# Kernel optimization log

Measured on AMD Instinct MI355X. Metric: run time of the kernel, lower is better.

The kernel has to match this reference:

```python
import jax, jax.numpy as jnp
import numpy as np

H = 8
D_MODEL = 512
D_K = D_MODEL // H
NEG = -1e9


def setup_inputs() -> dict:
    key = jax.random.key(0)
    ks = jax.random.split(key, 11)
    B, S = 2, 2048
    scale = 1.0 / np.sqrt(D_MODEL)
    inp = {
        'query': jax.random.normal(ks[0], (B, S, D_MODEL), dtype=jnp.float32),
        'key': jax.random.normal(ks[1], (B, S, D_MODEL), dtype=jnp.float32),
        'value': jax.random.normal(ks[2], (B, S, D_MODEL), dtype=jnp.float32),
        'Wq': jax.random.normal(ks[3], (D_MODEL, D_MODEL), dtype=jnp.float32) * scale,
        'bq': jnp.zeros((D_MODEL,), dtype=jnp.float32),
        'Wk': jax.random.normal(ks[4], (D_MODEL, D_MODEL), dtype=jnp.float32) * scale,
        'bk': jnp.zeros((D_MODEL,), dtype=jnp.float32),
        'Wv': jax.random.normal(ks[5], (D_MODEL, D_MODEL), dtype=jnp.float32) * scale,
        'bv': jnp.zeros((D_MODEL,), dtype=jnp.float32),
        'Wo': jax.random.normal(ks[6], (D_MODEL, D_MODEL), dtype=jnp.float32) * scale,
        'bo': jnp.zeros((D_MODEL,), dtype=jnp.float32),
    }
    return inp


def reference(query, key, value, Wq, bq, Wk, bk, Wv, bv, Wo, bo):
    B, S, _ = query.shape
    # QKV projections (nn.Linear: x @ W.T + b), split into heads -> [B, H, S, D_K]
    def proj(x, W, b):
        return (x @ W.T + b).reshape(B, S, H, D_K).transpose(0, 2, 1, 3)

    q = proj(query, Wq, bq)
    k = proj(key, Wk, bk)
    v = proj(value, Wv, bv)

    scores = jnp.einsum('bhqd,bhkd->bhqk', q, k) / jnp.sqrt(jnp.float32(D_K))
    # diagonal mask (mask=True): token cannot attend to itself
    diag = jnp.eye(S, dtype=bool)
    scores = jnp.where(diag, NEG, scores)

    p_attn = jax.nn.softmax(scores, axis=-1)  # [B, H, S, S]
    x = jnp.einsum('bhqk,bhkd->bhqd', p_attn, v)
    x = x.transpose(0, 2, 1, 3).reshape(B, S, H * D_K)
    return x @ Wo.T + bo
```

## Files before the change

### kernel.cpp

```cpp
#include <hip/hip_runtime.h>
#include <hip/hip_bf16.h>
#include <math.h>

#define NUM_H 8
#define DK    64
#define DM    512
#define SEQ   2048
#define NB    2
#define MROWS (NB*SEQ)

typedef unsigned short u16;
typedef unsigned int   u32;
typedef __attribute__((ext_vector_type(8))) __bf16 bf16x8;
typedef __attribute__((ext_vector_type(4))) short  s16x4;
typedef __attribute__((ext_vector_type(4))) float  f32x4;

__device__ __forceinline__ u16 f2bf(float v) {
    union { __bf16 h; u16 u; } x; x.h = (__bf16)v; return x.u;
}
__device__ __forceinline__ u16 f2h(float v) {
    union { _Float16 h; u16 u; } x; x.h = (_Float16)v; return x.u;
}
__device__ __forceinline__ float h2f(u16 u) {
    union { u16 u; _Float16 h; } x; x.u = u; return (float)x.h;
}
__device__ __forceinline__ bf16x8 ld_bf8(const u16* p) {
    union { uint4 u; bf16x8 v; } t;
    t.u = *(const uint4*)p;
    return t.v;
}
__device__ __forceinline__ uint4 pack8bf(const float* f) {
    uint4 o;
    o.x = (u32)f2bf(f[0]) | ((u32)f2bf(f[1]) << 16);
    o.y = (u32)f2bf(f[2]) | ((u32)f2bf(f[3]) << 16);
    o.z = (u32)f2bf(f[4]) | ((u32)f2bf(f[5]) << 16);
    o.w = (u32)f2bf(f[6]) | ((u32)f2bf(f[7]) << 16);
    return o;
}

__device__ __forceinline__ f32x4 mfma16bf(s16x4 a, s16x4 b, f32x4 c) {
#if defined(__has_builtin) && __has_builtin(__builtin_amdgcn_mfma_f32_16x16x16bf16_1k)
    return __builtin_amdgcn_mfma_f32_16x16x16bf16_1k(a, b, c, 0, 0, 0);
#else
    asm("v_mfma_f32_16x16x16_bf16 %0, %1, %2, %0" : "+v"(c) : "v"(a), "v"(b));
    return c;
#endif
}

__global__ __launch_bounds__(256) void convW(
    const float* __restrict__ Wq, const float* __restrict__ Wk,
    const float* __restrict__ Wv, const float* __restrict__ Wo,
    u16* __restrict__ Wscr)
{
    const int z = blockIdx.y;
    const float* src = (z == 0) ? Wq : (z == 1) ? Wk : (z == 2) ? Wv : Wo;
    u16* dst = Wscr + (size_t)z * 262144;
    int i = (blockIdx.x * 256 + threadIdx.x) * 8;
    float4 a = *(const float4*)(src + i);
    float4 b = *(const float4*)(src + i + 4);
    float f[8] = {a.x, a.y, a.z, a.w, b.x, b.y, b.z, b.w};
    *(uint4*)&dst[i] = pack8bf(f);
}

#define MODE_QK 0
#define MODE_VT 1
#define MODE_FIN 2

template<int MODE, bool INBF>
__device__ __forceinline__ void gemm_core(
    const void* __restrict__ Xv, const u16* __restrict__ Wb,
    const float* __restrict__ bias, void* __restrict__ outv,
    u16* As, u16* Bs, int row0, int col0)
{
    const int tid = threadIdx.x;
    const int lane = tid & 63, w = tid >> 6;
    const int ln15 = lane & 15, quad = lane >> 4;
    const int wm = (w >> 1) * 32, wn = (w & 1) * 32;

    f32x4 acc[2][2];
#pragma unroll
    for (int mt = 0; mt < 2; ++mt)
#pragma unroll
        for (int nt = 0; nt < 2; ++nt) acc[mt][nt] = (f32x4){0.f, 0.f, 0.f, 0.f};

    for (int kt = 0; kt < DM; kt += 64) {
        __syncthreads();
#pragma unroll
        for (int g = 0; g < 2; ++g) {
            int idx = g * 2048 + tid * 8;
            int r = idx >> 6, c = idx & 63;
            if (INBF) {
                *(uint4*)&As[r * 72 + c] =
                    *(const uint4*)((const u16*)Xv + (size_t)(row0 + r) * DM + kt + c);
            } else {
                const float* xp = (const float*)Xv + (size_t)(row0 + r) * DM + kt + c;
                float4 a = *(const float4*)xp;
                float4 b2 = *(const float4*)(xp + 4);
                float f[8] = {a.x, a.y, a.z, a.w, b2.x, b2.y, b2.z, b2.w};
                *(uint4*)&As[r * 72 + c] = pack8bf(f);
            }
        }
#pragma unroll
        for (int g = 0; g < 2; ++g) {
            int idx = g * 2048 + tid * 8;
            int r = idx >> 6, c = idx & 63;
            *(uint4*)&Bs[r * 72 + c] =
                *(const uint4*)(Wb + (size_t)(col0 + r) * DM + kt + c);
        }
        __syncthreads();

#pragma unroll
        for (int ks = 0; ks < 2; ++ks) {
            bf16x8 af[2], bfr[2];
#pragma unroll
            for (int mt = 0; mt < 2; ++mt)
                af[mt] = ld_bf8(&As[(wm + mt * 16 + ln15) * 72 + ks * 32 + quad * 8]);
#pragma unroll
            for (int nt = 0; nt < 2; ++nt)
                bfr[nt] = ld_bf8(&Bs[(wn + nt * 16 + ln15) * 72 + ks * 32 + quad * 8]);
#pragma unroll
            for (int mt = 0; mt < 2; ++mt)
#pragma unroll
                for (int nt = 0; nt < 2; ++nt)
                    acc[mt][nt] = __builtin_amdgcn_mfma_f32_16x16x32_bf16(
                        af[mt], bfr[nt], acc[mt][nt], 0, 0, 0);
        }
    }

    float bc[2];
#pragma unroll
    for (int nt = 0; nt < 2; ++nt) bc[nt] = bias[col0 + wn + nt * 16 + ln15];
    const int h = col0 >> 6;

    if (MODE == MODE_FIN) {
        float* outF = (float*)outv;
#pragma unroll
        for (int mt = 0; mt < 2; ++mt)
#pragma unroll
            for (int r = 0; r < 4; ++r) {
                int m = row0 + wm + mt * 16 + quad * 4 + r;
#pragma unroll
                for (int nt = 0; nt < 2; ++nt)
                    outF[(size_t)m * DM + col0 + wn + nt * 16 + ln15] = acc[mt][nt][r] + bc[nt];
            }
    } else if (MODE == MODE_QK) {
        u16* outB = (u16*)outv;
#pragma unroll
        for (int mt = 0; mt < 2; ++mt)
#pragma unroll
            for (int r = 0; r < 4; ++r) {
                int m = row0 + wm + mt * 16 + quad * 4 + r;
                int b = m >> 11, s2 = m & (SEQ - 1);
#pragma unroll
                for (int nt = 0; nt < 2; ++nt) {
                    int dk = wn + nt * 16 + ln15;
                    outB[((size_t)((b * NUM_H + h) * SEQ + s2)) * DK + dk] =
                        f2bf(acc[mt][nt][r] + bc[nt]);
                }
            }
    } else {
        u16* outB = (u16*)outv;
        __syncthreads();
#pragma unroll
        for (int mt = 0; mt < 2; ++mt)
#pragma unroll
            for (int nt = 0; nt < 2; ++nt) {
                int dk = wn + nt * 16 + ln15;
#pragma unroll
                for (int r = 0; r < 4; ++r) {
                    int sl = wm + mt * 16 + quad * 4 + r;
                    As[dk * 72 + sl] = f2bf(acc[mt][nt][r] + bc[nt]);
                }
            }
        __syncthreads();
        int dk = tid >> 2, ch = (tid & 3) * 16;
        int b = row0 >> 11, s0 = row0 & (SEQ - 1);
        size_t base = ((size_t)((b * NUM_H + h) * DK + dk)) * SEQ + s0 + ch;
        *(uint4*)&outB[base]     = *(const uint4*)&As[dk * 72 + ch];
        *(uint4*)&outB[base + 8] = *(const uint4*)&As[dk * 72 + ch + 8];
    }
}

__global__ __launch_bounds__(256) void qkv_mfma(
    const float* __restrict__ xq, const float* __restrict__ xk, const float* __restrict__ xv,
    const u16* __restrict__ Wscr,
    const float* __restrict__ b0, const float* __restrict__ b1, const float* __restrict__ b2,
    u16* __restrict__ oQ, u16* __restrict__ oK, u16* __restrict__ oVt)
{
    __shared__ u16 As[64 * 72];
    __shared__ u16 Bs[64 * 72];
    const int row0 = blockIdx.x * 64, col0 = blockIdx.y * 64;
    const int z = blockIdx.z;
    const u16* W = Wscr + (size_t)z * 262144;
    if (z == 2)
        gemm_core<MODE_VT, false>(xv, W, b2, oVt, As, Bs, row0, col0);
    else if (z == 0)
        gemm_core<MODE_QK, false>(xq, W, b0, oQ, As, Bs, row0, col0);
    else
        gemm_core<MODE_QK, false>(xk, W, b1, oK, As, Bs, row0, col0);
}

__global__ __launch_bounds__(256) void final_mfma(
    const u16* __restrict__ X, const u16* __restrict__ Wbf,
    const float* __restrict__ bias, float* __restrict__ out)
{
    __shared__ u16 As[64 * 72];
    __shared__ u16 Bs[64 * 72];
    gemm_core<MODE_FIN, true>(X, Wbf, bias, out, As, Bs,
                              blockIdx.x * 64, blockIdx.y * 64);
}

#define LSTR 72
__global__ __launch_bounds__(256) void attn_mfma(
    const u16* __restrict__ Qg, const u16* __restrict__ Kg,
    const u16* __restrict__ Vtg, u16* __restrict__ Pd, float* __restrict__ Cl)
{
    __shared__ u16 Klds[64 * LSTR];
    __shared__ u16 Vtlds[64 * LSTR];

    const int tid = threadIdx.x;
    const int lane = tid & 63;
    const int w = tid >> 6;
    const int ln15 = lane & 15;
    const int quad = lane >> 4;
    const int bh = blockIdx.y;
    const int b = bh >> 3, h = bh & 7;
    const int qb = blockIdx.x * 64;
    const int z = blockIdx.z;
    const int k0 = z * (SEQ / 2), k1 = k0 + SEQ / 2;

    const u16* Qp = Qg + (size_t)bh * SEQ * DK;
    const u16* Kp = Kg + (size_t)bh * SEQ * DK;
    const u16* Vp = Vtg + (size_t)bh * DK * SEQ;

    const int myq = w * 16 + ln15;
    const int qrow = qb + myq;
    const bf16x8 qa0 = ld_bf8(&Qp[(size_t)qrow * DK + quad * 8]);
    const bf16x8 qa1 = ld_bf8(&Qp[(size_t)qrow * DK + 32 + quad * 8]);

    f32x4 O[4];
    float lsum = 0.f;
#pragma unroll
    for (int nt = 0; nt < 4; ++nt) O[nt] = (f32x4){0.f, 0.f, 0.f, 0.f};

    const int sr = tid >> 3;
    const int scl = (tid & 7) * 8;

    for (int kt = k0; kt < k1; kt += 64) {
        __syncthreads();
        *(uint4*)&Klds[sr * LSTR + scl]         = *(const uint4*)&Kp[(size_t)(kt + sr) * DK + scl];
        *(uint4*)&Klds[(sr + 32) * LSTR + scl]  = *(const uint4*)&Kp[(size_t)(kt + sr + 32) * DK + scl];
        *(uint4*)&Vtlds[sr * LSTR + scl]        = *(const uint4*)&Vp[(size_t)sr * SEQ + kt + scl];
        *(uint4*)&Vtlds[(sr + 32) * LSTR + scl] = *(const uint4*)&Vp[(size_t)(sr + 32) * SEQ + kt + scl];
        __syncthreads();

        const bool diagt = (kt == qb);
        s16x4 pa[4];
#pragma unroll
        for (int nt2 = 0; nt2 < 4; ++nt2) {
            bf16x8 kb0 = ld_bf8(&Klds[(nt2 * 16 + ln15) * LSTR + quad * 8]);
            bf16x8 kb1 = ld_bf8(&Klds[(nt2 * 16 + ln15) * LSTR + 32 + quad * 8]);
            f32x4 zacc = (f32x4){0.f, 0.f, 0.f, 0.f};
            zacc = __builtin_amdgcn_mfma_f32_16x16x32_bf16(kb0, qa0, zacc, 0, 0, 0);
            zacc = __builtin_amdgcn_mfma_f32_16x16x32_bf16(kb1, qa1, zacc, 0, 0, 0);
            union { u16 u[4]; s16x4 v; } pk;
#pragma unroll
            for (int r = 0; r < 4; ++r) {
                float e = __expf(fmaf(zacc[r], 0.125f, -4.0f));
                if (diagt && (nt2 * 16 + quad * 4 + r == myq)) e = 0.f;
                lsum += e;
                pk.u[r] = f2bf(e);
            }
            pa[nt2] = pk.v;
        }

        const u16* vb_base = &Vtlds[ln15 * LSTR + quad * 4];
#pragma unroll
        for (int nt = 0; nt < 4; ++nt) {
#pragma unroll
            for (int nt2 = 0; nt2 < 4; ++nt2) {
                s16x4 vb = *(const s16x4*)&vb_base[nt * 16 * LSTR + nt2 * 16];
                O[nt] = mfma16bf(pa[nt2], vb, O[nt]);
            }
        }
    }

    lsum += __shfl_xor(lsum, 16);
    lsum += __shfl_xor(lsum, 32);
    if (quad == 0)
        Cl[(size_t)z * 32768 + bh * SEQ + qb + myq] = lsum;

#pragma unroll
    for (int r = 0; r < 4; ++r) {
        int s = qb + w * 16 + quad * 4 + r;
        size_t base = (size_t)z * 2097152 + ((size_t)(b * SEQ + s)) * DM + h * DK;
#pragma unroll
        for (int nt = 0; nt < 4; ++nt)
            Pd[base + nt * 16 + ln15] = f2h(O[nt][r] * 0.015625f);
    }
}

__global__ __launch_bounds__(256) void combine(
    const u16* __restrict__ Pd, const float* __restrict__ Cl, u16* __restrict__ C)
{
    int idx = (blockIdx.x * 256 + threadIdx.x) * 8;
    int row = idx >> 9, col = idx & 511;
    int b = row >> 11, s = row & (SEQ - 1), h = col >> 6;
    int bh = b * NUM_H + h;
    float lsum = Cl[bh * SEQ + s] + Cl[32768 + bh * SEQ + s];
    float sc = 64.f / lsum;
    uint4 u0 = *(const uint4*)&Pd[idx];
    uint4 u1 = *(const uint4*)&Pd[2097152 + idx];
    u32 a0[4] = {u0.x, u0.y, u0.z, u0.w};
    u32 a1[4] = {u1.x, u1.y, u1.z, u1.w};
    float f[8];
#pragma unroll
    for (int j = 0; j < 4; ++j) {
        f[2 * j]     = (h2f((u16)(a0[j] & 0xffff)) + h2f((u16)(a1[j] & 0xffff))) * sc;
        f[2 * j + 1] = (h2f((u16)(a0[j] >> 16))    + h2f((u16)(a1[j] >> 16)))    * sc;
    }
    *(uint4*)&C[idx] = pack8bf(f);
}

extern "C" void kernel_launch(void* const* d_in, const int* in_sizes, int n_in,
                              void* d_out, int out_size, void* d_ws, size_t ws_size,
                              hipStream_t stream) {
    const float* q  = (const float*)d_in[0];
    const float* k  = (const float*)d_in[1];
    const float* v  = (const float*)d_in[2];
    const float* Wq = (const float*)d_in[3];
    const float* bq = (const float*)d_in[4];
    const float* Wk = (const float*)d_in[5];
    const float* bk = (const float*)d_in[6];
    const float* Wv = (const float*)d_in[7];
    const float* bv = (const float*)d_in[8];
    const float* Wo = (const float*)d_in[9];
    const float* bo = (const float*)d_in[10];
    float* out = (float*)d_out;

    const size_t TSZ = (size_t)MROWS * DM;
    u16* Qb  = (u16*)d_ws;
    u16* Kb  = Qb + TSZ;
    u16* Vtb = Qb + 2 * TSZ;
    u16* CbU = Qb + 3 * TSZ;
    float* Cl  = (float*)CbU;
    u16*  Wscr = CbU + 131072;

    u16* Pd = (u16*)d_out;

    dim3 blk(256);
    hipLaunchKernelGGL(convW, dim3(128, 4), blk, 0, stream, Wq, Wk, Wv, Wo, Wscr);
    dim3 gq(MROWS / 64, DM / 64, 3);
    hipLaunchKernelGGL(qkv_mfma, gq, blk, 0, stream,
                       q, k, v, Wscr, bq, bk, bv, Qb, Kb, Vtb);
    dim3 ga(SEQ / 64, NB * NUM_H, 2);
    hipLaunchKernelGGL(attn_mfma, ga, blk, 0, stream, Qb, Kb, Vtb, Pd, Cl);
    hipLaunchKernelGGL(combine, dim3(1024), blk, 0, stream, Pd, Cl, Qb);
    dim3 gf(MROWS / 64, DM / 64);
    hipLaunchKernelGGL(final_mfma, gf, blk, 0, stream, Qb, Wscr + 3 * 262144, bo, out);
}
```

Measured before the change: 160.7 us.

## Prefetch K/V tiles into registers, compute row sums via MFMA, use exp2

The attention loop now loads the next K and V tile from global memory into registers while the current tile is being computed. The LDS store happens at the top of each iteration with a single barrier. Row sums of P are no longer accumulated with scalar adds and shuffles; they come from an extra MFMA against a ones vector, which also makes the sum use the same bf16-rounded probabilities as the P·V product. The exponential uses a native exp2 with constants pre-scaled by log2(e), the diagonal mask is applied only on the tile that contains it, and s_setprio raises wave priority around the MFMA block. The cost is more registers for the prefetch buffers and a small change in rounding.

```diff
diff --git a/kernel.cpp b/kernel.cpp
--- a/kernel.cpp
+++ b/kernel.cpp
@@ -36,6 +36,13 @@
     o.z = (u32)f2bf(f[4]) | ((u32)f2bf(f[5]) << 16);
     o.w = (u32)f2bf(f[6]) | ((u32)f2bf(f[7]) << 16);
     return o;
+}
+__device__ __forceinline__ float fexp2(float x) {
+#if defined(__has_builtin) && __has_builtin(__builtin_amdgcn_exp2f)
+    return __builtin_amdgcn_exp2f(x);
+#else
+    return exp2f(x);
+#endif
 }
 
 __device__ __forceinline__ f32x4 mfma16bf(s16x4 a, s16x4 b, f32x4 c) {
@@ -211,6 +218,8 @@
 }
 
 #define LSTR 72
+#define SCL2  0.18033688f
+#define BIA2 -5.7708020f
 __global__ __launch_bounds__(256) void attn_mfma(
     const u16* __restrict__ Qg, const u16* __restrict__ Kg,
     const u16* __restrict__ Vtg, u16* __restrict__ Pd, float* __restrict__ Cl)
@@ -238,21 +247,42 @@
     const bf16x8 qa0 = ld_bf8(&Qp[(size_t)qrow * DK + quad * 8]);
     const bf16x8 qa1 = ld_bf8(&Qp[(size_t)qrow * DK + 32 + quad * 8]);
 
+    const bool mrow = (quad == (ln15 >> 2));
+    const int  mr   = ln15 & 3;
+
+    const s16x4 onesb = (s16x4){(short)0x3F80, (short)0x3F80,
+                                (short)0x3F80, (short)0x3F80};
+
     f32x4 O[4];
-    float lsum = 0.f;
+    f32x4 Lacc = (f32x4){0.f, 0.f, 0.f, 0.f};
 #pragma unroll
     for (int nt = 0; nt < 4; ++nt) O[nt] = (f32x4){0.f, 0.f, 0.f, 0.f};
 
     const int sr = tid >> 3;
     const int scl = (tid & 7) * 8;
+    const u16* kp0 = &Kp[(size_t)sr * DK + scl];
+    const u16* kp1 = &Kp[(size_t)(sr + 32) * DK + scl];
+    const u16* vp0 = &Vp[(size_t)sr * SEQ + scl];
+    const u16* vp1 = &Vp[(size_t)(sr + 32) * SEQ + scl];
+
+    uint4 kreg0 = *(const uint4*)&kp0[(size_t)k0 * DK];
+    uint4 kreg1 = *(const uint4*)&kp1[(size_t)k0 * DK];
+    uint4 vreg0 = *(const uint4*)&vp0[k0];
+    uint4 vreg1 = *(const uint4*)&vp1[k0];
 
     for (int kt = k0; kt < k1; kt += 64) {
-        __syncthreads();
-        *(uint4*)&Klds[sr * LSTR + scl]         = *(const uint4*)&Kp[(size_t)(kt + sr) * DK + scl];
-        *(uint4*)&Klds[(sr + 32) * LSTR + scl]  = *(const uint4*)&Kp[(size_t)(kt + sr + 32) * DK + scl];
-        *(uint4*)&Vtlds[sr * LSTR + scl]        = *(const uint4*)&Vp[(size_t)sr * SEQ + kt + scl];
-        *(uint4*)&Vtlds[(sr + 32) * LSTR + scl] = *(const uint4*)&Vp[(size_t)(sr + 32) * SEQ + kt + scl];
-        __syncthreads();
+        *(uint4*)&Klds[sr * LSTR + scl]         = kreg0;
+        *(uint4*)&Klds[(sr + 32) * LSTR + scl]  = kreg1;
+        *(uint4*)&Vtlds[sr * LSTR + scl]        = vreg0;
+        *(uint4*)&Vtlds[(sr + 32) * LSTR + scl] = vreg1;
+        __syncthreads();
+
+        if (kt + 64 < k1) {
+            kreg0 = *(const uint4*)&kp0[(size_t)(kt + 64) * DK];
+            kreg1 = *(const uint4*)&kp1[(size_t)(kt + 64) * DK];
+            vreg0 = *(const uint4*)&vp0[kt + 64];
+            vreg1 = *(const uint4*)&vp1[kt + 64];
+        }
 
         const bool diagt = (kt == qb);
         s16x4 pa[4];
@@ -265,16 +295,21 @@
             zacc = __builtin_amdgcn_mfma_f32_16x16x32_bf16(kb1, qa1, zacc, 0, 0, 0);
             union { u16 u[4]; s16x4 v; } pk;
 #pragma unroll
-            for (int r = 0; r < 4; ++r) {
-                float e = __expf(fmaf(zacc[r], 0.125f, -4.0f));
-                if (diagt && (nt2 * 16 + quad * 4 + r == myq)) e = 0.f;
-                lsum += e;
-                pk.u[r] = f2bf(e);
+            for (int r = 0; r < 4; ++r)
+                pk.u[r] = f2bf(fexp2(fmaf(zacc[r], SCL2, BIA2)));
+            if (diagt && nt2 == w) {
+#pragma unroll
+                for (int r = 0; r < 4; ++r)
+                    if (mrow && r == mr) pk.u[r] = 0;
             }
             pa[nt2] = pk.v;
         }
 
         const u16* vb_base = &Vtlds[ln15 * LSTR + quad * 4];
+        __builtin_amdgcn_s_setprio(1);
+#pragma unroll
+        for (int nt2 = 0; nt2 < 4; ++nt2)
+            Lacc = mfma16bf(pa[nt2], onesb, Lacc);
 #pragma unroll
         for (int nt = 0; nt < 4; ++nt) {
 #pragma unroll
@@ -283,12 +318,15 @@
                 O[nt] = mfma16bf(pa[nt2], vb, O[nt]);
             }
         }
-    }
-
-    lsum += __shfl_xor(lsum, 16);
-    lsum += __shfl_xor(lsum, 32);
-    if (quad == 0)
-        Cl[(size_t)z * 32768 + bh * SEQ + qb + myq] = lsum;
+        __builtin_amdgcn_s_setprio(0);
+        __syncthreads();
+    }
+
+    if (ln15 == 0) {
+#pragma unroll
+        for (int r = 0; r < 4; ++r)
+            Cl[(size_t)z * 32768 + bh * SEQ + qb + w * 16 + quad * 4 + r] = Lacc[r];
+    }
 
 #pragma unroll
     for (int r = 0; r < 4; ++r) {
```

New measurement: 151.9 us. -5.5%, faster.
